# Optimization experiments

Hardware: AMD Instinct MI355X
Metric: run time of the kernel (lower is better)

The kernel has to match this reference:

```python
import jax, jax.numpy as jnp
import numpy as np

N, L, S, D, H = 2, 2048, 2048, 128, 32  # batch, query len, state len, hidden_dim(=head dim), num_heads


def setup_inputs() -> dict:
    key = jax.random.key(0)
    ks = jax.random.split(key, 8)
    return {
        "query": jax.random.normal(ks[0], (N, L, D), dtype=jnp.float32),
        "states": jax.random.normal(ks[1], (N, S, D), dtype=jnp.float32),
        "Wk": jax.random.normal(ks[2], (H, D, D), dtype=jnp.float32) * 0.05,
        "bk": jax.random.normal(ks[3], (H, D), dtype=jnp.float32) * 0.05,
        "Wv": jax.random.normal(ks[4], (H, D, D), dtype=jnp.float32) * 0.05,
        "bv": jax.random.normal(ks[5], (H, D), dtype=jnp.float32) * 0.05,
        "Wc": jax.random.normal(ks[6], (H * D, D), dtype=jnp.float32) * 0.02,
        "bc": jax.random.normal(ks[7], (D,), dtype=jnp.float32) * 0.02,
    }


def reference(query, states, Wk, bk, Wv, bv, Wc, bc):
    # Per-head key/value projections (Attention.keys_mlp / values_mlp), batched over heads.
    K = jnp.einsum('nsd,hdk->nhsk', states, Wk) + bk[None, :, None, :]  # [N,H,S,D]
    V = jnp.einsum('nsd,hdk->nhsk', states, Wv) + bv[None, :, None, :]  # [N,H,S,D]
    scale = jnp.sqrt(jnp.asarray(K.shape[-1], query.dtype))
    logits = jnp.einsum('nld,nhsd->nhls', query, K) / scale            # [N,H,L,S]
    # Original detaches attention scores (softmax(...).detach()).
    A = jax.lax.stop_gradient(jax.nn.softmax(logits, axis=-1))
    ctx = jnp.einsum('nhls,nhsd->nhld', A, V)                          # [N,H,L,D]
    n, h, l, d = ctx.shape
    ctx = ctx.transpose(0, 2, 1, 3).reshape(n, l, h * d)               # concat heads -> [N,L,H*D]
    return ctx @ Wc + bc                                               # context_transform
```

## Files before the change

### kernel.cpp

```cpp
#include <hip/hip_runtime.h>
#include <hip/hip_bf16.h>

#define N_B 2
#define L_Q 2048
#define S_S 2048
#define D_D 128
#define H_H 32
#define SCALEK (0.08838834764831845f * 1.4426950408889634f)

typedef __attribute__((ext_vector_type(8))) short bf8;
typedef __attribute__((ext_vector_type(4))) short bf4;
typedef __attribute__((ext_vector_type(4))) float f4;

#define MFMA(a, b, c) __builtin_amdgcn_mfma_f32_16x16x32_bf16(a, b, c, 0, 0, 0)

__device__ __forceinline__ short f2bf(float x) {
    union { float f; unsigned u; } v; v.f = x;
    unsigned r = v.u + 0x7FFFu + ((v.u >> 16) & 1u);
    return (short)(r >> 16);
}

__device__ __forceinline__ bf4 pk4(float a, float b, float c, float d) {
    union { __hip_bfloat162 h2[2]; bf4 v; } u;
    u.h2[0] = __float22bfloat162_rn(make_float2(a, b));
    u.h2[1] = __float22bfloat162_rn(make_float2(c, d));
    return u.v;
}

__device__ __forceinline__ bf8 cat44(bf4 lo, bf4 hi) {
    bf8 r;
    r[0] = lo[0]; r[1] = lo[1]; r[2] = lo[2]; r[3] = lo[3];
    r[4] = hi[0]; r[5] = hi[1]; r[6] = hi[2]; r[7] = hi[3];
    return r;
}

__device__ __forceinline__ bf8 load8(const float* p) {
    const float4* q = (const float4*)p;
    float4 a = q[0], b = q[1];
    bf8 r;
    r[0] = f2bf(a.x); r[1] = f2bf(a.y); r[2] = f2bf(a.z); r[3] = f2bf(a.w);
    r[4] = f2bf(b.x); r[5] = f2bf(b.y); r[6] = f2bf(b.z); r[7] = f2bf(b.w);
    return r;
}

__device__ __forceinline__ void async16(const void* g, void* l) {
    __builtin_amdgcn_global_load_lds(
        (const __attribute__((address_space(1))) unsigned*)g,
        (__attribute__((address_space(3))) unsigned*)l, 16, 0, 0);
}

__global__ __launch_bounds__(256) void k_wct(const float* __restrict__ Wc,
                                             unsigned short* __restrict__ WcT) {
    int idx = blockIdx.x * 256 + threadIdx.x;
    int n = idx >> 12;
    int k = idx & 4095;
    WcT[idx] = (unsigned short)f2bf(Wc[k * D_D + n]);
}

__global__ __launch_bounds__(256) void k_proj(const float* __restrict__ states,
        const float* __restrict__ Wk, const float* __restrict__ bk,
        const float* __restrict__ Wv, const float* __restrict__ bv,
        unsigned short* __restrict__ Kb, unsigned short* __restrict__ VTb) {
    __shared__ unsigned short WT[128 * 128];
    const int tid = threadIdx.x;
    const int l = tid & 63, w = tid >> 6;
    const int lrow = l & 15, lgrp = l >> 4;
    const int bx = blockIdx.x;
    const int sc = bx & 31;
    const int nh = bx >> 5;
    const int h = nh & 31, n = nh >> 5;
    const int job = blockIdx.y;

    const float* W = (job ? Wv : Wk) + (size_t)h * (D_D * D_D);
    char* WTc = (char*)WT;
    #pragma unroll
    for (int i = 0; i < 64; ++i) {
        int flat = i * 256 + tid;
        int k = flat >> 7, d = flat & 127;
        short val = f2bf(W[flat]);
        int off = d * 256 + ((k * 2) ^ ((d & 7) << 4));
        *(short*)(WTc + off) = val;
    }
    __syncthreads();

    if (job == 0) {
        const float* srow = states + ((size_t)n * S_S + sc * 64 + w * 16 + lrow) * D_D;
        bf8 a[4];
        #pragma unroll
        for (int t = 0; t < 4; ++t) a[t] = load8(srow + t * 32 + lgrp * 8);
        f4 acc[8];
        #pragma unroll
        for (int i = 0; i < 8; ++i) acc[i] = (f4)(0.f);
        #pragma unroll
        for (int nf = 0; nf < 8; ++nf) {
            int drow = nf * 16 + lrow;
            int swz = (drow & 7) << 4;
            #pragma unroll
            for (int t = 0; t < 4; ++t) {
                bf8 b = *(const bf8*)(WTc + drow * 256 + (((t * 32 + lgrp * 8) * 2) ^ swz));
                acc[nf] = MFMA(a[t], b, acc[nf]);
            }
        }
        unsigned short* Kout = Kb + (size_t)(n * H_H + h) * S_S * D_D;
        #pragma unroll
        for (int nf = 0; nf < 8; ++nf) {
            int dcol = nf * 16 + lrow;
            float bias = bk[h * D_D + dcol];
            #pragma unroll
            for (int r = 0; r < 4; ++r) {
                int srw = sc * 64 + w * 16 + lgrp * 4 + r;
                Kout[(size_t)srw * D_D + dcol] = (unsigned short)f2bf((acc[nf][r] + bias) * SCALEK);
            }
        }
    } else {
        bf8 a[2][4];
        #pragma unroll
        for (int mf = 0; mf < 2; ++mf) {
            int drow = w * 32 + mf * 16 + lrow;
            int swz = (drow & 7) << 4;
            #pragma unroll
            for (int t = 0; t < 4; ++t)
                a[mf][t] = *(const bf8*)(WTc + drow * 256 + (((t * 32 + lgrp * 8) * 2) ^ swz));
        }
        f4 acc[2][4];
        #pragma unroll
        for (int mf = 0; mf < 2; ++mf)
            #pragma unroll
            for (int nf = 0; nf < 4; ++nf) acc[mf][nf] = (f4)(0.f);
        #pragma unroll
        for (int nf = 0; nf < 4; ++nf) {
            const float* srow = states + ((size_t)n * S_S + sc * 64 + nf * 16 + lrow) * D_D;
            #pragma unroll
            for (int t = 0; t < 4; ++t) {
                bf8 b = load8(srow + t * 32 + lgrp * 8);
                acc[0][nf] = MFMA(a[0][t], b, acc[0][nf]);
                acc[1][nf] = MFMA(a[1][t], b, acc[1][nf]);
            }
        }
        unsigned short* Vout = VTb + (size_t)(n * H_H + h) * D_D * S_S;
        #pragma unroll
        for (int mf = 0; mf < 2; ++mf) {
            #pragma unroll
            for (int r = 0; r < 4; ++r) {
                int drow = w * 32 + mf * 16 + lgrp * 4 + r;
                float bias = bv[h * D_D + drow];
                #pragma unroll
                for (int nf = 0; nf < 4; ++nf) {
                    int p = ((nf >> 1) << 5) + ((lrow >> 2) << 3) + ((nf & 1) << 2) + (lrow & 3);
                    int scol = sc * 64 + p;
                    Vout[(size_t)drow * S_S + scol] = (unsigned short)f2bf(acc[mf][nf][r] + bias);
                }
            }
        }
    }
}

__global__ __launch_bounds__(256) void k_attn(const float* __restrict__ query,
        const unsigned short* __restrict__ Kb, const unsigned short* __restrict__ VTb,
        unsigned short* __restrict__ CTX) {
    __shared__ char smem[65536];
    const int tid = threadIdx.x;
    const int l = tid & 63, w = tid >> 6;
    const int lrow = l & 15, lgrp = l >> 4;

    const int bid = blockIdx.x;
    const int bx = (bid & 7) * 128 + (bid >> 3);
    const int qt = bx & 15;
    const int nh = bx >> 4;
    const int h = nh & 31, n = nh >> 5;
    const int qbase = qt * 128 + w * 32;

    bf8 qf[2][4];
    #pragma unroll
    for (int mf = 0; mf < 2; ++mf) {
        const float* qp = query + ((size_t)n * L_Q + qbase + mf * 16 + lrow) * D_D;
        #pragma unroll
        for (int t = 0; t < 4; ++t) qf[mf][t] = load8(qp + t * 32 + lgrp * 8);
    }

    f4 oacc[2][8];
    #pragma unroll
    for (int mf = 0; mf < 2; ++mf)
        #pragma unroll
        for (int df = 0; df < 8; ++df) oacc[mf][df] = (f4)(0.f);
    float rsum[2] = {0.f, 0.f};

    const char* Kg = (const char*)(Kb + (size_t)(n * H_H + h) * S_S * D_D);
    const char* Vg = (const char*)(VTb + (size_t)(n * H_H + h) * D_D * S_S);

    auto stage = [&](int c, int sc2) {
        char* Kl = smem + c * 16384;
        char* Vl = smem + 32768 + c * 16384;
        #pragma unroll
        for (int rnd = 0; rnd < 4; ++rnd) {
            int o = w * 4096 + rnd * 1024 + l * 16;
            int r = o >> 8;
            int b = (o & 255) ^ ((r & 7) << 4);
            async16(Kg + (size_t)(sc2 * 64 + r) * 256 + b, Kl + w * 4096 + rnd * 1024);
        }
        #pragma unroll
        for (int rnd = 0; rnd < 4; ++rnd) {
            int o = w * 4096 + rnd * 1024 + l * 16;
            int r = o >> 7;
            int b = (o & 127) ^ ((r & 7) << 4);
            async16(Vg + (size_t)r * 4096 + sc2 * 128 + b, Vl + w * 4096 + rnd * 1024);
        }
    };

    stage(0, 0);
    __syncthreads();
    int cur = 0;

    for (int sc2 = 0; sc2 < 32; ++sc2) {
        if (sc2 < 31) stage(cur ^ 1, sc2 + 1);
        const char* Klds = smem + cur * 16384;
        const char* Vlds = smem + 32768 + cur * 16384;

        f4 sacc[2][4];
        #pragma unroll
        for (int mf = 0; mf < 2; ++mf)
            #pragma unroll
            for (int nf = 0; nf < 4; ++nf) sacc[mf][nf] = (f4)(0.f);
        __builtin_amdgcn_s_setprio(1);
        #pragma unroll
        for (int nf = 0; nf < 4; ++nf) {
            int srow = nf * 16 + lrow;
            int swz = (srow & 7) << 4;
            #pragma unroll
            for (int t = 0; t < 4; ++t) {
                bf8 kb = *(const bf8*)(Klds + srow * 256 + (((t * 32 + lgrp * 8) * 2) ^ swz));
                sacc[0][nf] = MFMA(kb, qf[0][t], sacc[0][nf]);
                sacc[1][nf] = MFMA(kb, qf[1][t], sacc[1][nf]);
            }
        }
        __builtin_amdgcn_s_setprio(0);

        bf8 pf[2][2];
        #pragma unroll
        for (int mf = 0; mf < 2; ++mf) {
            #pragma unroll
            for (int g = 0; g < 2; ++g) {
                bf4 pblk[2];
                #pragma unroll
                for (int b2 = 0; b2 < 2; ++b2) {
                    int nf = g * 2 + b2;
                    float p0 = __builtin_amdgcn_exp2f(sacc[mf][nf][0]);
                    float p1 = __builtin_amdgcn_exp2f(sacc[mf][nf][1]);
                    float p2 = __builtin_amdgcn_exp2f(sacc[mf][nf][2]);
                    float p3 = __builtin_amdgcn_exp2f(sacc[mf][nf][3]);
                    rsum[mf] += (p0 + p1) + (p2 + p3);
                    pblk[b2] = pk4(p0, p1, p2, p3);
                }
                pf[mf][g] = cat44(pblk[0], pblk[1]);
            }
        }

        __builtin_amdgcn_s_setprio(1);
        #pragma unroll
        for (int df = 0; df < 8; ++df) {
            int drow = df * 16 + lrow;
            int swz = (drow & 7) << 4;
            #pragma unroll
            for (int g = 0; g < 2; ++g) {
                bf8 vf = *(const bf8*)(Vlds + drow * 128 + ((g * 64 + lgrp * 16) ^ swz));
                oacc[0][df] = MFMA(vf, pf[0][g], oacc[0][df]);
                oacc[1][df] = MFMA(vf, pf[1][g], oacc[1][df]);
            }
        }
        __builtin_amdgcn_s_setprio(0);

        __syncthreads();
        cur ^= 1;
    }

    float rinv[2];
    #pragma unroll
    for (int mf = 0; mf < 2; ++mf) {
        float v = rsum[mf];
        v += __shfl_xor(v, 16, 64);
        v += __shfl_xor(v, 32, 64);
        rinv[mf] = 1.f / v;
    }
    #pragma unroll
    for (int mf = 0; mf < 2; ++mf) {
        int qrow = qbase + mf * 16 + lrow;
        unsigned short* crow = CTX + (size_t)(n * L_Q + qrow) * 4096 + h * D_D;
        #pragma unroll
        for (int df = 0; df < 8; ++df) {
            bf4 o = pk4(oacc[mf][df][0] * rinv[mf], oacc[mf][df][1] * rinv[mf],
                        oacc[mf][df][2] * rinv[mf], oacc[mf][df][3] * rinv[mf]);
            *(bf4*)(crow + df * 16 + lgrp * 4) = o;
        }
    }
}

__global__ __launch_bounds__(256) void k_out(const unsigned short* __restrict__ CTX,
        const unsigned short* __restrict__ WcT, const float* __restrict__ bc,
        float* __restrict__ out) {
    __shared__ char Alds[8192];
    const int tid = threadIdx.x;
    const int l = tid & 63, w = tid >> 6;
    const int lrow = l & 15, lgrp = l >> 4;
    const int m0 = blockIdx.x * 16;
    const char* Ag = (const char*)(CTX + (size_t)m0 * 4096);

    auto stage = [&](int c, int kc) {
        int o = w * 1024 + l * 16;
        int r = o >> 8;
        int b = (o & 255) ^ ((r & 7) << 4);
        async16(Ag + (size_t)r * 8192 + kc * 256 + b, Alds + c * 4096 + w * 1024);
    };

    f4 acc[2];
    acc[0] = (f4)(0.f); acc[1] = (f4)(0.f);
    stage(0, 0);
    __syncthreads();
    int cur = 0;
    for (int kc = 0; kc < 32; ++kc) {
        if (kc < 31) stage(cur ^ 1, kc + 1);
        const char* Ac = Alds + cur * 4096;
        #pragma unroll
        for (int t = 0; t < 4; ++t) {
            int swz = (lrow & 7) << 4;
            bf8 a = *(const bf8*)(Ac + lrow * 256 + (((t * 32 + lgrp * 8) * 2) ^ swz));
            #pragma unroll
            for (int nf = 0; nf < 2; ++nf) {
                int nc = w * 32 + nf * 16 + lrow;
                bf8 b = *(const bf8*)(WcT + (size_t)nc * 4096 + kc * 128 + t * 32 + lgrp * 8);
                acc[nf] = MFMA(a, b, acc[nf]);
            }
        }
        __syncthreads();
        cur ^= 1;
    }
    #pragma unroll
    for (int nf = 0; nf < 2; ++nf) {
        int nc = w * 32 + nf * 16 + lrow;
        float bias = bc[nc];
        #pragma unroll
        for (int r = 0; r < 4; ++r)
            out[(size_t)(m0 + lgrp * 4 + r) * D_D + nc] = acc[nf][r] + bias;
    }
}

extern "C" void kernel_launch(void* const* d_in, const int* in_sizes, int n_in,
                              void* d_out, int out_size, void* d_ws, size_t ws_size,
                              hipStream_t stream) {
    const float* query  = (const float*)d_in[0];
    const float* states = (const float*)d_in[1];
    const float* Wk = (const float*)d_in[2];
    const float* bk = (const float*)d_in[3];
    const float* Wv = (const float*)d_in[4];
    const float* bv = (const float*)d_in[5];
    const float* Wc = (const float*)d_in[6];
    const float* bc = (const float*)d_in[7];
    float* out = (float*)d_out;

    char* ws = (char*)d_ws;
    unsigned short* Kb  = (unsigned short*)(ws);
    unsigned short* VTb = (unsigned short*)(ws + 33554432);
    unsigned short* CTX = (unsigned short*)(ws + 67108864);
    unsigned short* WcT = (unsigned short*)(ws + 100663296);

    k_wct<<<2048, 256, 0, stream>>>(Wc, WcT);
    dim3 gb(2048, 2);
    k_proj<<<gb, 256, 0, stream>>>(states, Wk, bk, Wv, bv, Kb, VTb);
    k_attn<<<1024, 256, 0, stream>>>(query, Kb, VTb, CTX);
    k_out<<<256, 256, 0, stream>>>(CTX, WcT, bc, out);
}
```

Baseline: 266.9 us.

## Pretranspose K/V weights once, drop per-block LDS transpose, unroll attention loop

Adds a small kernel that converts Wk/Wv to bf16 and transposes them once into workspace, aliased onto the CTX buffer region before CTX is written. k_proj then reads the transposed weights directly from global memory instead of having each of its 4096 blocks redo the fp32 to bf16 transpose into LDS. The attention kernel also gets a launch-bounds occupancy hint of 2 and a main loop unrolled by two so the buffer indices become compile-time constants. The trade-off is one extra launch and k_proj fetching weight fragments from global or L2 rather than LDS.

```diff
diff --git a/kernel.cpp b/kernel.cpp
--- a/kernel.cpp
+++ b/kernel.cpp
@@ -57,11 +57,37 @@
     WcT[idx] = (unsigned short)f2bf(Wc[k * D_D + n]);
 }
 
+__global__ __launch_bounds__(256) void k_wt(const float* __restrict__ Wk,
+        const float* __restrict__ Wv, unsigned short* __restrict__ WkT,
+        unsigned short* __restrict__ WvT) {
+    __shared__ unsigned short T[128][129];
+    const int tid = threadIdx.x;
+    const int h = blockIdx.x;
+    const int job = blockIdx.y;
+    const float* W = (job ? Wv : Wk) + (size_t)h * (D_D * D_D);
+    unsigned short* WT = (job ? WvT : WkT) + (size_t)h * (D_D * D_D);
+
+    #pragma unroll
+    for (int i = 0; i < 64; ++i) {
+        int flat = i * 256 + tid;
+        T[flat >> 7][flat & 127] = (unsigned short)f2bf(W[flat]);
+    }
+    __syncthreads();
+    #pragma unroll
+    for (int j8 = 0; j8 < 8; ++j8) {
+        int idx = j8 * 256 + tid;
+        int d = idx >> 4, k0 = (idx & 15) * 8;
+        bf8 v;
+        #pragma unroll
+        for (int j = 0; j < 8; ++j) v[j] = (short)T[k0 + j][d];
+        *(bf8*)(WT + d * D_D + k0) = v;
+    }
+}
+
 __global__ __launch_bounds__(256) void k_proj(const float* __restrict__ states,
-        const float* __restrict__ Wk, const float* __restrict__ bk,
-        const float* __restrict__ Wv, const float* __restrict__ bv,
+        const unsigned short* __restrict__ WkT, const float* __restrict__ bk,
+        const unsigned short* __restrict__ WvT, const float* __restrict__ bv,
         unsigned short* __restrict__ Kb, unsigned short* __restrict__ VTb) {
-    __shared__ unsigned short WT[128 * 128];
     const int tid = threadIdx.x;
     const int l = tid & 63, w = tid >> 6;
     const int lrow = l & 15, lgrp = l >> 4;
@@ -71,19 +97,8 @@
     const int h = nh & 31, n = nh >> 5;
     const int job = blockIdx.y;
 
-    const float* W = (job ? Wv : Wk) + (size_t)h * (D_D * D_D);
-    char* WTc = (char*)WT;
-    #pragma unroll
-    for (int i = 0; i < 64; ++i) {
-        int flat = i * 256 + tid;
-        int k = flat >> 7, d = flat & 127;
-        short val = f2bf(W[flat]);
-        int off = d * 256 + ((k * 2) ^ ((d & 7) << 4));
-        *(short*)(WTc + off) = val;
-    }
-    __syncthreads();
-
     if (job == 0) {
+        const unsigned short* WT = WkT + (size_t)h * (D_D * D_D);
         const float* srow = states + ((size_t)n * S_S + sc * 64 + w * 16 + lrow) * D_D;
         bf8 a[4];
         #pragma unroll
@@ -94,10 +109,9 @@
         #pragma unroll
         for (int nf = 0; nf < 8; ++nf) {
             int drow = nf * 16 + lrow;
-            int swz = (drow & 7) << 4;
             #pragma unroll
             for (int t = 0; t < 4; ++t) {
-                bf8 b = *(const bf8*)(WTc + drow * 256 + (((t * 32 + lgrp * 8) * 2) ^ swz));
+                bf8 b = *(const bf8*)(WT + drow * D_D + t * 32 + lgrp * 8);
                 acc[nf] = MFMA(a[t], b, acc[nf]);
             }
         }
@@ -113,14 +127,14 @@
             }
         }
     } else {
+        const unsigned short* WT = WvT + (size_t)h * (D_D * D_D);
         bf8 a[2][4];
         #pragma unroll
         for (int mf = 0; mf < 2; ++mf) {
             int drow = w * 32 + mf * 16 + lrow;
-            int swz = (drow & 7) << 4;
             #pragma unroll
             for (int t = 0; t < 4; ++t)
-                a[mf][t] = *(const bf8*)(WTc + drow * 256 + (((t * 32 + lgrp * 8) * 2) ^ swz));
+                a[mf][t] = *(const bf8*)(WT + drow * D_D + t * 32 + lgrp * 8);
         }
         f4 acc[2][4];
         #pragma unroll
@@ -155,7 +169,7 @@
     }
 }
 
-__global__ __launch_bounds__(256) void k_attn(const float* __restrict__ query,
+__global__ __launch_bounds__(256, 2) void k_attn(const float* __restrict__ query,
         const unsigned short* __restrict__ Kb, const unsigned short* __restrict__ VTb,
         unsigned short* __restrict__ CTX) {
     __shared__ char smem[65536];
@@ -207,12 +221,8 @@
         }
     };
 
-    stage(0, 0);
-    __syncthreads();
-    int cur = 0;
-
-    for (int sc2 = 0; sc2 < 32; ++sc2) {
-        if (sc2 < 31) stage(cur ^ 1, sc2 + 1);
+    auto iter = [&](int cur, int sc2, bool prefetch) {
+        if (prefetch) stage(cur ^ 1, sc2 + 1);
         const char* Klds = smem + cur * 16384;
         const char* Vlds = smem + 32768 + cur * 16384;
 
@@ -268,9 +278,14 @@
             }
         }
         __builtin_amdgcn_s_setprio(0);
-
         __syncthreads();
-        cur ^= 1;
+    };
+
+    stage(0, 0);
+    __syncthreads();
+    for (int s2 = 0; s2 < 32; s2 += 2) {
+        iter(0, s2, true);
+        iter(1, s2 + 1, s2 + 1 < 31);
     }
 
     float rinv[2];
@@ -360,11 +375,15 @@
     unsigned short* Kb  = (unsigned short*)(ws);
     unsigned short* VTb = (unsigned short*)(ws + 33554432);
     unsigned short* CTX = (unsigned short*)(ws + 67108864);
+    unsigned short* WkT = (unsigned short*)(ws + 67108864);
+    unsigned short* WvT = (unsigned short*)(ws + 67108864 + 1048576);
     unsigned short* WcT = (unsigned short*)(ws + 100663296);
 
     k_wct<<<2048, 256, 0, stream>>>(Wc, WcT);
+    dim3 gw(32, 2);
+    k_wt<<<gw, 256, 0, stream>>>(Wk, Wv, WkT, WvT);
     dim3 gb(2048, 2);
-    k_proj<<<gb, 256, 0, stream>>>(states, Wk, bk, Wv, bv, Kb, VTb);
+    k_proj<<<gb, 256, 0, stream>>>(states, WkT, bk, WvT, bv, Kb, VTb);
     k_attn<<<1024, 256, 0, stream>>>(query, Kb, VTb, CTX);
     k_out<<<256, 256, 0, stream>>>(CTX, WcT, bc, out);
 }
```

Result: slower. 276.5 us (+3.6%).
